# Performance work log

Hardware: AMD Instinct MI355X
Metric: run time of the kernel (lower is better)

The kernel has to match this reference:

```python
import jax, jax.numpy as jnp
import numpy as np

K = 5            # spline kernel size per dim
NUM_CLASSES = 10
EPS = 1e-4       # matches module's normalize eps
ROUTING_ITERS = 3
_BITS = jnp.array([[(b >> 2) & 1, (b >> 1) & 1, b & 1] for b in range(8)], dtype=jnp.float32)  # [8,3]


def normalize(t, axis=-1):
    return t / (jnp.sqrt(jnp.sum(t * t, axis=axis, keepdims=True)) + EPS)


def quat_mul(q, r):
    # quaternions stored (x, y, z, w) -- module sets identity as [:,:,:,3]=1
    qx, qy, qz, qw = q[..., 0], q[..., 1], q[..., 2], q[..., 3]
    rx, ry, rz, rw = r[..., 0], r[..., 1], r[..., 2], r[..., 3]
    return jnp.stack([
        qw * rx + qx * rw + qy * rz - qz * ry,
        qw * ry - qx * rz + qy * rw + qz * rx,
        qw * rz + qx * ry - qy * rx + qz * rw,
        qw * rw - qx * rx - qy * ry - qz * rz,
    ], axis=-1)


def spline_conv(x, pseudo, src, dst, W, root, bias, n_nodes):
    # degree-1 open B-spline conv, kernel 5^3, in=1, out=16
    v = pseudo * (K - 1)                                   # [E,3]
    i0 = jnp.clip(jnp.floor(v), 0, K - 2)                  # [E,3]
    frac = v - i0
    i0 = i0.astype(jnp.int32)
    idx = i0[:, None, :] + _BITS.astype(jnp.int32)[None]   # [E,8,3]
    kflat = (idx[..., 0] * K + idx[..., 1]) * K + idx[..., 2]  # [E,8]
    wb = jnp.prod(jnp.where(_BITS[None] > 0, frac[:, None, :], 1.0 - frac[:, None, :]), axis=-1)  # [E,8]
    Wg = W[kflat]                                          # [E,8,16] irregular gather (dominant traffic)
    wk = jnp.einsum('eb,ebo->eo', wb, Wg)                  # [E,16]
    msg = x[src] * wk                                      # [E,16] (in-channels = 1)
    agg = jax.ops.segment_sum(msg, dst, num_segments=n_nodes)
    deg = jax.ops.segment_sum(jnp.ones_like(dst, dtype=x.dtype), dst, num_segments=n_nodes)
    return agg / jnp.maximum(deg, 1.0)[:, None] + x @ root + bias


def caps_layer(pose, act, q):
    # pose [N,I,4], act [N,I], q [I,J,4] -> pose [N,J,4], act [N,J]
    qn = normalize(q)
    pred = normalize(quat_mul(qn[None], pose[:, :, None, :]))  # [N,I,J,4]
    b = jnp.zeros(pred.shape[:3], dtype=pose.dtype)
    for _ in range(ROUTING_ITERS):
        c = jax.nn.softmax(b, axis=2) * act[:, :, None]
        s = jnp.einsum('nij,nijq->njq', c, pred)
        v = normalize(s)
        b = b + jnp.einsum('nijq,njq->nij', pred, v)
    act_out = jax.nn.sigmoid(jnp.einsum('nij,nijq,njq->nj', c, pred, v))
    return v, act_out


def pool_by_agreement(pose, act, pos, G, start, size):
    # voxel-grid clustering + agreement-weighted quaternion averaging
    g = jnp.clip(jnp.floor((pos - start) / size), 0, G - 1).astype(jnp.int32)  # [N,3]
    vid = (g[:, 0] * G + g[:, 1]) * G + g[:, 2]
    V = G ** 3
    s = jax.ops.segment_sum(act[:, :, None] * pose, vid, num_segments=V)  # [V,J,4]
    m = normalize(s)
    agree = jnp.sum(pose * m[vid], axis=-1)                                # [N,J]
    wsum = jax.ops.segment_sum(act, vid, num_segments=V)
    cnt = jax.ops.segment_sum(jnp.ones((pose.shape[0],), pose.dtype), vid, num_segments=V)
    act_out = jax.nn.sigmoid(jax.ops.segment_sum(act * agree, vid, num_segments=V) / (wsum + EPS))
    pos_out = jax.ops.segment_sum(pos, vid, num_segments=V) / (cnt[:, None] + EPS)
    return m, act_out, pos_out


def forward(x, pos, pseudo, W_spline, root, bias, lin_w, lin_b, q0, q1, q3, q5, q6, q7, edge_index):
    N = x.shape[0]
    src, dst = edge_index[0], edge_index[1]
    h = spline_conv(x, pseudo, src, dst, W_spline, root, bias, N)   # [N,16]
    quats = jax.nn.elu(h) @ lin_w + lin_b                           # [N,4]
    pose = normalize(quats.reshape(N, 1, 4))                        # [N,1,4]
    act = x.reshape(N, 1)                                           # expand to num_caps_in=1
    pose, act = caps_layer(pose, act, q0)                           # 1 -> 6
    pose, act = caps_layer(pose, act, q1)                           # 6 -> 6
    min_pos, max_pos = pos.min(), pos.max()
    rng = max_pos + 0.001 - min_pos
    pose, act, p = pool_by_agreement(pose, act, pos, 32, min_pos, rng / 32)   # -> 32768 voxels
    pose, act = caps_layer(pose, act, q3)                           # 6 -> 8
    pose, act, p = pool_by_agreement(pose, act, p, 8, min_pos, rng / 8)       # -> 512
    pose, act = caps_layer(pose, act, q5)                           # 8 -> 12
    pose, act, p = pool_by_agreement(pose, act, p, 2, min_pos, rng / 2)       # -> 8
    pose, act = caps_layer(pose, act, q6)                           # 12 -> 14
    pose, act, p = pool_by_agreement(pose, act, p, 1, min_pos - 0.5, max_pos - min_pos + 1.0)  # -> 1
    pose, act = caps_layer(pose, act, q7)                           # 14 -> 10
    return act                                                      # [1, 10]


def setup_inputs() -> dict:
    key = jax.random.key(0)
    ks = jax.random.split(key, 16)
    N, E = 50000, 800000
    def caps_q(k, i, j):
        return jax.random.normal(k, (i, j, 4), dtype=jnp.float32)
    return {
        'x': jax.random.uniform(ks[0], (N, 1), dtype=jnp.float32),
        'pos': jax.random.uniform(ks[1], (N, 3), dtype=jnp.float32),
        'pseudo': jax.random.uniform(ks[2], (E, 3), dtype=jnp.float32),
        'W_spline': jax.random.normal(ks[3], (K ** 3, 16), dtype=jnp.float32) * 0.1,
        'root': jax.random.normal(ks[4], (1, 16), dtype=jnp.float32) * 0.1,
        'bias': jnp.zeros((16,), dtype=jnp.float32),
        'lin_w': jax.random.normal(ks[5], (16, 4), dtype=jnp.float32) * 0.25,
        'lin_b': jnp.zeros((4,), dtype=jnp.float32),
        'q0': caps_q(ks[6], 1, 6),
        'q1': caps_q(ks[7], 6, 6),
        'q3': caps_q(ks[8], 6, 8),
        'q5': caps_q(ks[9], 8, 12),
        'q6': caps_q(ks[10], 12, 14),
        'q7': caps_q(ks[11], 14, NUM_CLASSES),
        'edge_index': jax.random.randint(ks[12], (2, E), 0, N, dtype=jnp.int32),
    }


def reference(x, pos, pseudo, W_spline, root, bias, lin_w, lin_b, q0, q1, q3, q5, q6, q7, edge_index):
    return forward(x, pos, pseudo, W_spline, root, bias, lin_w, lin_b, q0, q1, q3, q5, q6, q7, edge_index)
```

## Files before the change

### kernel.cpp

```cpp
#include <hip/hip_runtime.h>
#include <math.h>

#define EPS 1e-4f

__device__ __forceinline__ float sigmoidf_(float x){ return 1.0f/(1.0f+expf(-x)); }

__device__ __forceinline__ unsigned f2u_(float f){
    unsigned u = __float_as_uint(f);
    return (u & 0x80000000u) ? ~u : (u | 0x80000000u);
}
__device__ __forceinline__ float u2f_(unsigned u){
    unsigned b = (u & 0x80000000u) ? (u & 0x7FFFFFFFu) : ~u;
    return __uint_as_float(b);
}

__global__ void minmax_kernel(const float* __restrict__ p, int n, unsigned* mm){
    float lo = INFINITY, hi = -INFINITY;
    for (int i = blockIdx.x*blockDim.x + threadIdx.x; i < n; i += gridDim.x*blockDim.x){
        float v = p[i]; lo = fminf(lo, v); hi = fmaxf(hi, v);
    }
    for (int off = 32; off > 0; off >>= 1){
        lo = fminf(lo, __shfl_down(lo, off));
        hi = fmaxf(hi, __shfl_down(hi, off));
    }
    __shared__ float slo[8], shi[8];
    int wid = threadIdx.x >> 6;
    if ((threadIdx.x & 63) == 0){ slo[wid] = lo; shi[wid] = hi; }
    __syncthreads();
    if (threadIdx.x == 0){
        int nw = blockDim.x >> 6;
        for (int w = 1; w < nw; w++){ lo = fminf(lo, slo[w]); hi = fmaxf(hi, shi[w]); }
        atomicMin(&mm[0], f2u_(lo));
        atomicMax(&mm[1], f2u_(hi));
    }
}

__global__ void edge_rank(const int* __restrict__ ei, int* __restrict__ deg,
                          int* __restrict__ rank, int E){
    int e = blockIdx.x*blockDim.x + threadIdx.x;
    if (e >= E) return;
    rank[e] = atomicAdd(&deg[ei[E + e]], 1);
}

__global__ __launch_bounds__(256)
void scan_bsum(const int* __restrict__ deg, int* __restrict__ bsum, int N){
    int i = blockIdx.x*256 + threadIdx.x;
    int v = (i < N) ? deg[i] : 0;
    for (int o = 32; o > 0; o >>= 1) v += __shfl_down(v, o);
    __shared__ int ws[4];
    if ((threadIdx.x & 63) == 0) ws[threadIdx.x >> 6] = v;
    __syncthreads();
    if (threadIdx.x == 0) bsum[blockIdx.x] = ws[0] + ws[1] + ws[2] + ws[3];
}

__global__ __launch_bounds__(1024)
void scan_top(int* __restrict__ bsum, int NB){
    __shared__ int sh[1024];
    int t = threadIdx.x;
    int v = (t < NB) ? bsum[t] : 0;
    sh[t] = v;
    __syncthreads();
    for (int d = 1; d < 1024; d <<= 1){
        int u = (t >= d) ? sh[t - d] : 0;
        __syncthreads();
        sh[t] += u;
        __syncthreads();
    }
    if (t < NB) bsum[t] = sh[t] - v;
    if (t == 1023) bsum[NB] = sh[1023];
}

__global__ __launch_bounds__(256)
void scan_final(const int* __restrict__ deg, const int* __restrict__ bsum,
                int* __restrict__ off, int N, int NB){
    __shared__ int sh[256];
    int b = blockIdx.x;
    int i = b*256 + threadIdx.x;
    int v = (i < N) ? deg[i] : 0;
    sh[threadIdx.x] = v;
    __syncthreads();
    for (int d = 1; d < 256; d <<= 1){
        int u = (threadIdx.x >= d) ? sh[threadIdx.x - d] : 0;
        __syncthreads();
        sh[threadIdx.x] += u;
        __syncthreads();
    }
    if (i < N) off[i] = bsum[b] + sh[threadIdx.x] - v;
    if (b == 0 && threadIdx.x == 0) off[N] = bsum[NB];
}

__global__ void edge_pack(const int* __restrict__ ei, const float* __restrict__ pseudo,
                          const float* __restrict__ x,
                          const int* __restrict__ rank, const int* __restrict__ off,
                          float4* __restrict__ rec4, int* __restrict__ recb, int E){
    int e = blockIdx.x*blockDim.x + threadIdx.x;
    if (e >= E) return;
    float p0 = pseudo[3*e], p1 = pseudo[3*e+1], p2 = pseudo[3*e+2];
    int s = ei[e], d = ei[E + e];
    float v0 = p0*4.f, v1 = p1*4.f, v2 = p2*4.f;
    float f0 = fminf(fmaxf(floorf(v0), 0.f), 3.f);
    float f1 = fminf(fmaxf(floorf(v1), 0.f), 3.f);
    float f2 = fminf(fmaxf(floorf(v2), 0.f), 3.f);
    int slot = off[d] + rank[e];
    rec4[slot] = make_float4(v0 - f0, v1 - f1, v2 - f2, x[s]);
    recb[slot] = ((int)f0*5 + (int)f1)*5 + (int)f2;
}

__device__ __forceinline__ int voxel_id(const float* __restrict__ pos, int n, int G,
                                        float start, float size){
    int g[3];
    #pragma unroll
    for (int k = 0; k < 3; k++){
        float gg = floorf((pos[(size_t)n*3 + k] - start) / size);
        gg = fminf(fmaxf(gg, 0.f), (float)(G - 1));
        g[k] = (int)gg;
    }
    return (g[0]*G + g[1])*G + g[2];
}

__device__ __forceinline__ void pool_geom(const unsigned* mm, int G, int mode,
                                          float& start, float& size){
    float mn = u2f_(mm[0]), mx = u2f_(mm[1]);
    if (mode == 0){ start = mn; size = (mx + 0.001f - mn) / (float)G; }
    else          { start = mn - 0.5f; size = mx - mn + 1.0f; }
}

__global__ void elist_node(const float* __restrict__ pos, int* __restrict__ head,
                           int* __restrict__ nxt, int N, int G, int mode,
                           const unsigned* __restrict__ mm){
    int n = blockIdx.x*blockDim.x + threadIdx.x;
    if (n >= N) return;
    float start, size; pool_geom(mm, G, mode, start, size);
    int v = voxel_id(pos, n, G, start, size);
    nxt[n] = atomicExch(&head[v], n);
}

__global__ __launch_bounds__(256)
void spline_node_kernel(const float* __restrict__ x, const float4* __restrict__ rec4,
                        const int* __restrict__ recb, const int* __restrict__ off,
                        const float* __restrict__ W,
                        const float* __restrict__ root, const float* __restrict__ bias,
                        const float* __restrict__ lin_w, const float* __restrict__ lin_b,
                        float* __restrict__ pose, float* __restrict__ act, int N){
    __shared__ float Ws[125*17];
    for (int i = threadIdx.x; i < 125*16; i += blockDim.x)
        Ws[(i >> 4)*17 + (i & 15)] = W[i];
    __syncthreads();
    int t = blockIdx.x*blockDim.x + threadIdx.x;
    int n = t >> 3;
    int k = t & 7;
    if (n >= N) return;

    int o0 = off[n], o1 = off[n+1];

    float agg[16];
    #pragma unroll
    for (int o = 0; o < 16; o++) agg[o] = 0.f;

    for (int s = o0 + k; s < o1; s += 8){
        float4 rv = rec4[s];
        int base = recb[s];
        float fr0 = rv.x, fr1 = rv.y, fr2 = rv.z, xv = rv.w;
        #pragma unroll
        for (int b = 0; b < 8; b++){
            int b0 = (b >> 2) & 1, b1 = (b >> 1) & 1, b2 = b & 1;
            float w = (b0 ? fr0 : 1.f - fr0) * (b1 ? fr1 : 1.f - fr1) * (b2 ? fr2 : 1.f - fr2);
            w *= xv;
            const float* Wr = &Ws[(base + b0*25 + b1*5 + b2)*17];
            #pragma unroll
            for (int o = 0; o < 16; o++) agg[o] += w * Wr[o];
        }
    }

    #pragma unroll
    for (int o = 0; o < 16; o++){
        agg[o] += __shfl_xor(agg[o], 1);
        agg[o] += __shfl_xor(agg[o], 2);
        agg[o] += __shfl_xor(agg[o], 4);
    }

    if (k != 0) return;

    float deg = fmaxf((float)(o1 - o0), 1.0f);
    float xs = x[n];
    float qv0 = lin_b[0], qv1 = lin_b[1], qv2 = lin_b[2], qv3 = lin_b[3];
    #pragma unroll
    for (int o = 0; o < 16; o++){
        float h = agg[o] / deg + xs * root[o] + bias[o];
        float e = (h > 0.f) ? h : expm1f(h);
        qv0 += e * lin_w[o*4 + 0];
        qv1 += e * lin_w[o*4 + 1];
        qv2 += e * lin_w[o*4 + 2];
        qv3 += e * lin_w[o*4 + 3];
    }
    float inv = 1.0f / (sqrtf(qv0*qv0 + qv1*qv1 + qv2*qv2 + qv3*qv3) + EPS);
    pose[(size_t)n*4 + 0] = qv0*inv;
    pose[(size_t)n*4 + 1] = qv1*inv;
    pose[(size_t)n*4 + 2] = qv2*inv;
    pose[(size_t)n*4 + 3] = qv3*inv;
    act[n] = xs;
}

template<int I, int J>
__global__ __launch_bounds__(256)
void caps_wave_kernel(const float* __restrict__ poseIn, const float* __restrict__ actIn,
                      const float* __restrict__ q,
                      float* __restrict__ poseOut, float* __restrict__ actOut, int N){
    __shared__ float qn[I*J*4];
    for (int t = threadIdx.x; t < I*J; t += blockDim.x){
        float qa=q[t*4], qb=q[t*4+1], qc=q[t*4+2], qd=q[t*4+3];
        float inv = 1.f/(sqrtf(qa*qa+qb*qb+qc*qc+qd*qd)+EPS);
        qn[t*4+0]=qa*inv; qn[t*4+1]=qb*inv; qn[t*4+2]=qc*inv; qn[t*4+3]=qd*inv;
    }
    __syncthreads();
    int tid = blockIdx.x*blockDim.x + threadIdx.x;
    int n = tid >> 3;
    int j = tid & 7;
    const bool on = (n < N) && (j < J);

    float pr[I][4], a[I], b[I];
    #pragma unroll
    for (int i = 0; i < I; i++){
        pr[i][0]=pr[i][1]=pr[i][2]=pr[i][3]=0.f; a[i]=0.f;
        b[i] = on ? 0.f : -INFINITY;
    }
    if (on){
        #pragma unroll
        for (int i = 0; i < I; i++){
            float4 p = *reinterpret_cast<const float4*>(&poseIn[((size_t)n*I + i)*4]);
            a[i] = actIn[(size_t)n*I + i];
            const float* qq = &qn[(i*J + j)*4];
            float qx=qq[0], qy=qq[1], qz=qq[2], qw=qq[3];
            float tx = qw*p.x + qx*p.w + qy*p.z - qz*p.y;
            float ty = qw*p.y - qx*p.z + qy*p.w + qz*p.x;
            float tz = qw*p.z + qx*p.y - qy*p.x + qz*p.w;
            float tw = qw*p.w - qx*p.x - qy*p.y - qz*p.z;
            float inv = 1.f/(sqrtf(tx*tx+ty*ty+tz*tz+tw*tw)+EPS);
            pr[i][0]=tx*inv; pr[i][1]=ty*inv; pr[i][2]=tz*inv; pr[i][3]=tw*inv;
        }
    }

    float c[I], v0=0.f, v1=0.f, v2=0.f, v3=0.f;
    #pragma unroll
    for (int t = 0; t < 3; t++){
        #pragma unroll
        for (int i = 0; i < I; i++){
            float mb = b[i];
            mb = fmaxf(mb, __shfl_xor(mb, 1));
            mb = fmaxf(mb, __shfl_xor(mb, 2));
            mb = fmaxf(mb, __shfl_xor(mb, 4));
            float e = on ? expf(b[i] - mb) : 0.f;
            float s = e;
            s += __shfl_xor(s, 1);
            s += __shfl_xor(s, 2);
            s += __shfl_xor(s, 4);
            c[i] = a[i] * e / s;
        }
        float s0=0.f, s1=0.f, s2=0.f, s3=0.f;
        #pragma unroll
        for (int i = 0; i < I; i++){
            s0 += c[i]*pr[i][0]; s1 += c[i]*pr[i][1];
            s2 += c[i]*pr[i][2]; s3 += c[i]*pr[i][3];
        }
        float inv = 1.f/(sqrtf(s0*s0+s1*s1+s2*s2+s3*s3)+EPS);
        v0=s0*inv; v1=s1*inv; v2=s2*inv; v3=s3*inv;
        if (t < 2){
            #pragma unroll
            for (int i = 0; i < I; i++)
                b[i] += pr[i][0]*v0 + pr[i][1]*v1 + pr[i][2]*v2 + pr[i][3]*v3;
        }
    }

    if (on){
        float acc = 0.f;
        #pragma unroll
        for (int i = 0; i < I; i++)
            acc += c[i]*(pr[i][0]*v0 + pr[i][1]*v1 + pr[i][2]*v2 + pr[i][3]*v3);
        actOut[(size_t)n*J + j] = sigmoidf_(acc);
        *reinterpret_cast<float4*>(&poseOut[((size_t)n*J + j)*4]) =
            make_float4(v0, v1, v2, v3);
    }
}

template<int I, int J, int NPB>
__global__ __launch_bounds__(NPB*I*J)
void caps_coop_kernel(const float* __restrict__ poseIn, const float* __restrict__ actIn,
                      const float* __restrict__ q, float* __restrict__ poseOut,
                      float* __restrict__ actOut, int N){
    const int IJ = I*J;
    const int tid = threadIdx.x;
    const int nl  = tid / IJ;
    const int li  = tid - nl*IJ;
    const int i   = li / J;
    const int j   = li - i*J;
    const int node = blockIdx.x*NPB + nl;
    const bool on = (node < N);

    __shared__ float redA[NPB][I*J];
    __shared__ float redB[NPB][I*J];
    __shared__ float cp[NPB][I*J*4];
    __shared__ float vsh[NPB][J*4];

    float prx=0.f, pry=0.f, prz=0.f, prw=0.f, ai=0.f;
    if (on){
        float qx = q[li*4+0], qy = q[li*4+1], qz = q[li*4+2], qw = q[li*4+3];
        float qinv = 1.0f/(sqrtf(qx*qx+qy*qy+qz*qz+qw*qw)+EPS);
        qx*=qinv; qy*=qinv; qz*=qinv; qw*=qinv;
        const float* pp = &poseIn[((size_t)node*I + i)*4];
        float rx=pp[0], ry=pp[1], rz=pp[2], rw=pp[3];
        ai = actIn[(size_t)node*I + i];
        float tx = qw*rx + qx*rw + qy*rz - qz*ry;
        float ty = qw*ry - qx*rz + qy*rw + qz*rx;
        float tz = qw*rz + qx*ry - qy*rx + qz*rw;
        float tw = qw*rw - qx*rx - qy*ry - qz*rz;
        float pinv = 1.0f/(sqrtf(tx*tx+ty*ty+tz*tz+tw*tw)+EPS);
        prx=tx*pinv; pry=ty*pinv; prz=tz*pinv; prw=tw*pinv;
    }

    float b = 0.f, c = 0.f;
    for (int t = 0; t < 3; t++){
        redA[nl][li] = b;
        __syncthreads();
        float mb = -INFINITY;
        #pragma unroll
        for (int jj = 0; jj < J; jj++) mb = fmaxf(mb, redA[nl][i*J+jj]);
        float e = expf(b - mb);
        redB[nl][li] = e;
        __syncthreads();
        float s = 0.f;
        #pragma unroll
        for (int jj = 0; jj < J; jj++) s += redB[nl][i*J+jj];
        c = ai * e / s;
        cp[nl][li*4+0] = c*prx; cp[nl][li*4+1] = c*pry;
        cp[nl][li*4+2] = c*prz; cp[nl][li*4+3] = c*prw;
        __syncthreads();
        for (int idx = li; idx < J*4; idx += IJ){
            int jj = idx >> 2, comp = idx & 3;
            float acc = 0.f;
            #pragma unroll
            for (int ii = 0; ii < I; ii++) acc += cp[nl][(ii*J+jj)*4+comp];
            vsh[nl][idx] = acc;
        }
        __syncthreads();
        if (li < J){
            float a0=vsh[nl][li*4], a1=vsh[nl][li*4+1], a2=vsh[nl][li*4+2], a3=vsh[nl][li*4+3];
            float inv = 1.0f/(sqrtf(a0*a0+a1*a1+a2*a2+a3*a3)+EPS);
            vsh[nl][li*4]=a0*inv; vsh[nl][li*4+1]=a1*inv;
            vsh[nl][li*4+2]=a2*inv; vsh[nl][li*4+3]=a3*inv;
        }
        __syncthreads();
        if (t < 2){
            b += prx*vsh[nl][j*4] + pry*vsh[nl][j*4+1] + prz*vsh[nl][j*4+2] + prw*vsh[nl][j*4+3];
            __syncthreads();
        } else {
            redA[nl][li] = c*(prx*vsh[nl][j*4] + pry*vsh[nl][j*4+1]
                            + prz*vsh[nl][j*4+2] + prw*vsh[nl][j*4+3]);
            __syncthreads();
            if (li < J && on){
                float acc = 0.f;
                #pragma unroll
                for (int ii = 0; ii < I; ii++) acc += redA[nl][ii*J+li];
                actOut[(size_t)node*J + li] = sigmoidf_(acc);
                poseOut[((size_t)node*J+li)*4+0] = vsh[nl][li*4+0];
                poseOut[((size_t)node*J+li)*4+1] = vsh[nl][li*4+1];
                poseOut[((size_t)node*J+li)*4+2] = vsh[nl][li*4+2];
                poseOut[((size_t)node*J+li)*4+3] = vsh[nl][li*4+3];
            }
        }
    }
}

template<int J>
__global__ __launch_bounds__(256)
void pool1_gather_kernel(const float* __restrict__ pose, const float* __restrict__ act,
                         const float* __restrict__ pos,
                         const int* __restrict__ head, const int* __restrict__ nxt,
                         float* __restrict__ poseOut, float* __restrict__ actOut,
                         float* __restrict__ posOut, int V){
    int v = blockIdx.x*blockDim.x + threadIdx.x;
    if (v >= V) return;

    float s[J][4], w[J], ps0=0.f, ps1=0.f, ps2=0.f;
    #pragma unroll
    for (int j = 0; j < J; j++){ s[j][0]=0.f; s[j][1]=0.f; s[j][2]=0.f; s[j][3]=0.f; w[j]=0.f; }

    int cnt = 0;
    for (int n = head[v]; n >= 0; n = nxt[n]){
        const float* pb = &pose[(size_t)n*J*4];
        const float* ab = &act[(size_t)n*J];
        #pragma unroll
        for (int j = 0; j < J; j++){
            float aj = ab[j];
            s[j][0] += aj*pb[j*4+0];
            s[j][1] += aj*pb[j*4+1];
            s[j][2] += aj*pb[j*4+2];
            s[j][3] += aj*pb[j*4+3];
            w[j] += aj;
        }
        ps0 += pos[(size_t)n*3+0];
        ps1 += pos[(size_t)n*3+1];
        ps2 += pos[(size_t)n*3+2];
        cnt++;
    }
    #pragma unroll
    for (int j = 0; j < J; j++){
        float inv = 1.0f/(sqrtf(s[j][0]*s[j][0]+s[j][1]*s[j][1]+
                                s[j][2]*s[j][2]+s[j][3]*s[j][3])+EPS);
        s[j][0]*=inv; s[j][1]*=inv; s[j][2]*=inv; s[j][3]*=inv;
    }
    float ag[J];
    #pragma unroll
    for (int j = 0; j < J; j++) ag[j] = 0.f;
    for (int n = head[v]; n >= 0; n = nxt[n]){
        const float* pb = &pose[(size_t)n*J*4];
        const float* ab = &act[(size_t)n*J];
        #pragma unroll
        for (int j = 0; j < J; j++){
            float agree = pb[j*4+0]*s[j][0] + pb[j*4+1]*s[j][1]
                        + pb[j*4+2]*s[j][2] + pb[j*4+3]*s[j][3];
            ag[j] += ab[j]*agree;
        }
    }
    #pragma unroll
    for (int j = 0; j < J; j++){
        size_t o = (size_t)v*J + j;
        actOut[o] = sigmoidf_(ag[j] / (w[j] + EPS));
        poseOut[o*4+0] = s[j][0];
        poseOut[o*4+1] = s[j][1];
        poseOut[o*4+2] = s[j][2];
        poseOut[o*4+3] = s[j][3];
    }
    float c = (float)cnt + EPS;
    posOut[(size_t)v*3+0] = ps0 / c;
    posOut[(size_t)v*3+1] = ps1 / c;
    posOut[(size_t)v*3+2] = ps2 / c;
}

template<int V, int J, int CH, int NCHUNK>
__global__ void pool_priv1(const float4* __restrict__ poseIn, const float* __restrict__ actIn,
                           const float* __restrict__ posIn,
                           float* __restrict__ s, float* __restrict__ wsum,
                           float* __restrict__ cnt, float* __restrict__ psum,
                           int N, int G, int mode, const unsigned* __restrict__ mm){
    __shared__ float s_[V*CH*4];
    __shared__ float wsum_[V*CH];
    __shared__ float cnt_[V];
    __shared__ float psum_[V*3];
    const int chunk = blockIdx.x % NCHUNK;
    const int slice = blockIdx.x / NCHUNK;
    const int nslices = gridDim.x / NCHUNK;
    const int c0 = chunk * CH;

    for (int t = threadIdx.x; t < V*CH*4; t += blockDim.x) s_[t] = 0.f;
    for (int t = threadIdx.x; t < V*CH; t += blockDim.x) wsum_[t] = 0.f;
    if (chunk == 0){
        for (int t = threadIdx.x; t < V; t += blockDim.x) cnt_[t] = 0.f;
        for (int t = threadIdx.x; t < V*3; t += blockDim.x) psum_[t] = 0.f;
    }
    __syncthreads();

    float start, size; pool_geom(mm, G, mode, start, size);
    int per = (N + nslices - 1) / nslices;
    int n0 = slice * per, n1 = min(N, n0 + per);

    for (int n = n0 + (int)threadIdx.x; n < n1; n += blockDim.x){
        int vid = voxel_id(posIn, n, G, start, size);
        #pragma unroll
        for (int jj = 0; jj < CH; jj++){
            int j = c0 + jj;
            float aj = actIn[(size_t)n*J + j];
            float4 p = poseIn[(size_t)n*J + j];
            int b = (vid*CH + jj)*4;
            atomicAdd(&s_[b+0], aj*p.x);
            atomicAdd(&s_[b+1], aj*p.y);
            atomicAdd(&s_[b+2], aj*p.z);
            atomicAdd(&s_[b+3], aj*p.w);
            atomicAdd(&wsum_[vid*CH + jj], aj);
        }
        if (chunk == 0){
            atomicAdd(&cnt_[vid], 1.0f);
            atomicAdd(&psum_[vid*3+0], posIn[(size_t)n*3+0]);
            atomicAdd(&psum_[vid*3+1], posIn[(size_t)n*3+1]);
            atomicAdd(&psum_[vid*3+2], posIn[(size_t)n*3+2]);
        }
    }
    __syncthreads();

    for (int t = threadIdx.x; t < V*CH*4; t += blockDim.x){
        float val = s_[t];
        if (val != 0.f){
            int v = t / (CH*4), r = t % (CH*4);
            atomicAdd(&s[((size_t)v*J + c0)*4 + r], val);
        }
    }
    for (int t = threadIdx.x; t < V*CH; t += blockDim.x){
        float val = wsum_[t];
        if (val != 0.f){
            int v = t / CH, jj = t % CH;
            atomicAdd(&wsum[(size_t)v*J + c0 + jj], val);
        }
    }
    if (chunk == 0){
        for (int t = threadIdx.x; t < V; t += blockDim.x)
            if (cnt_[t] != 0.f) atomicAdd(&cnt[t], cnt_[t]);
        for (int t = threadIdx.x; t < V*3; t += blockDim.x)
            if (psum_[t] != 0.f) atomicAdd(&psum[t], psum_[t]);
    }
}

template<int V, int J>
__global__ void pool_priv2(const float4* __restrict__ poseIn, const float* __restrict__ actIn,
                           const float* __restrict__ posIn, const float4* __restrict__ m,
                           float* __restrict__ agacc,
                           int N, int G, int mode, const unsigned* __restrict__ mm){
    __shared__ float ag_[V*J];
    for (int t = threadIdx.x; t < V*J; t += blockDim.x) ag_[t] = 0.f;
    __syncthreads();
    float start, size; pool_geom(mm, G, mode, start, size);
    int nslices = gridDim.x;
    int per = (N + nslices - 1) / nslices;
    int n0 = blockIdx.x * per, n1 = min(N, n0 + per);
    for (int n = n0 + (int)threadIdx.x; n < n1; n += blockDim.x){
        int vid = voxel_id(posIn, n, G, start, size);
        #pragma unroll
        for (int j = 0; j < J; j++){
            float4 p  = poseIn[(size_t)n*J + j];
            float4 mv = m[(size_t)vid*J + j];
            float agree = p.x*mv.x + p.y*mv.y + p.z*mv.z + p.w*mv.w;
            atomicAdd(&ag_[vid*J + j], actIn[(size_t)n*J + j]*agree);
        }
    }
    __syncthreads();
    for (int t = threadIdx.x; t < V*J; t += blockDim.x)
        if (ag_[t] != 0.f) atomicAdd(&agacc[t], ag_[t]);
}

__global__ void pool_m(const float* __restrict__ s, float* __restrict__ m, int VJ){
    int t = blockIdx.x*blockDim.x + threadIdx.x;
    if (t >= VJ) return;
    float a = s[(size_t)t*4], b = s[(size_t)t*4+1], c = s[(size_t)t*4+2], d = s[(size_t)t*4+3];
    float inv = 1.0f / (sqrtf(a*a + b*b + c*c + d*d) + EPS);
    m[(size_t)t*4]   = a*inv;
    m[(size_t)t*4+1] = b*inv;
    m[(size_t)t*4+2] = c*inv;
    m[(size_t)t*4+3] = d*inv;
}

__global__ void pool_fin(const float* __restrict__ agacc, const float* __restrict__ wsum,
                         const float* __restrict__ cnt, const float* __restrict__ psum,
                         float* __restrict__ actOut, float* __restrict__ posOut, int V, int J){
    int t = blockIdx.x*blockDim.x + threadIdx.x;
    if (t >= V*J) return;
    int v = t / J, j = t % J;
    actOut[t] = sigmoidf_(agacc[t] / (wsum[t] + EPS));
    if (j == 0){
        float c = cnt[v] + EPS;
        posOut[(size_t)v*3 + 0] = psum[(size_t)v*3 + 0] / c;
        posOut[(size_t)v*3 + 1] = psum[(size_t)v*3 + 1] / c;
        posOut[(size_t)v*3 + 2] = psum[(size_t)v*3 + 2] / c;
    }
}

template<int NIN, int J>
__global__ __launch_bounds__(64)
void pool4_tiny(const float* __restrict__ poseIn, const float* __restrict__ actIn,
                const float* __restrict__ posIn,
                float* __restrict__ poseOut, float* __restrict__ actOut,
                float* __restrict__ posOut){
    int t = threadIdx.x;
    if (t < J){
        float s0=0.f, s1=0.f, s2=0.f, s3=0.f, w=0.f;
        #pragma unroll
        for (int n = 0; n < NIN; n++){
            float a = actIn[n*J + t];
            const float* pb = &poseIn[(n*J + t)*4];
            s0 += a*pb[0]; s1 += a*pb[1]; s2 += a*pb[2]; s3 += a*pb[3];
            w += a;
        }
        float inv = 1.f/(sqrtf(s0*s0+s1*s1+s2*s2+s3*s3)+EPS);
        s0*=inv; s1*=inv; s2*=inv; s3*=inv;
        float ag = 0.f;
        #pragma unroll
        for (int n = 0; n < NIN; n++){
            float a = actIn[n*J + t];
            const float* pb = &poseIn[(n*J + t)*4];
            ag += a*(pb[0]*s0 + pb[1]*s1 + pb[2]*s2 + pb[3]*s3);
        }
        actOut[t] = sigmoidf_(ag / (w + EPS));
        poseOut[t*4+0]=s0; poseOut[t*4+1]=s1; poseOut[t*4+2]=s2; poseOut[t*4+3]=s3;
    } else if (t == J){
        float p0=0.f, p1=0.f, p2=0.f;
        #pragma unroll
        for (int n = 0; n < NIN; n++){
            p0 += posIn[n*3+0]; p1 += posIn[n*3+1]; p2 += posIn[n*3+2];
        }
        float c = (float)NIN + EPS;
        posOut[0]=p0/c; posOut[1]=p1/c; posOut[2]=p2/c;
    }
}

extern "C" void kernel_launch(void* const* d_in, const int* in_sizes, int n_in,
                              void* d_out, int out_size, void* d_ws, size_t ws_size,
                              hipStream_t stream){
    const float* x      = (const float*)d_in[0];
    const float* pos    = (const float*)d_in[1];
    const float* pseudo = (const float*)d_in[2];
    const float* Wsp    = (const float*)d_in[3];
    const float* root   = (const float*)d_in[4];
    const float* bias   = (const float*)d_in[5];
    const float* lin_w  = (const float*)d_in[6];
    const float* lin_b  = (const float*)d_in[7];
    const float* q0     = (const float*)d_in[8];
    const float* q1     = (const float*)d_in[9];
    const float* q3     = (const float*)d_in[10];
    const float* q5     = (const float*)d_in[11];
    const float* q6     = (const float*)d_in[12];
    const float* q7     = (const float*)d_in[13];
    const int*   ei     = (const int*)d_in[14];
    const int N = in_sizes[0];
    const int E = in_sizes[2] / 3;
    const int V1 = 32768;
    const int NB = (N + 255)/256;

    char* ws = (char*)d_ws;
    size_t off = 0;
    auto alloc = [&](size_t bytes)->void*{
        void* p = ws + off;
        off += (bytes + 255) & ~(size_t)255;
        return p;
    };
    unsigned* mm   = (unsigned*)alloc(8);
    int* deg       = (int*)alloc((size_t)N*sizeof(int));
    int* erank     = (int*)alloc((size_t)E*sizeof(int));
    int* eoff      = (int*)alloc((size_t)(N+1)*sizeof(int));
    int* bsum      = (int*)alloc((size_t)(NB+1)*sizeof(int));
    float4* rec4   = (float4*)alloc((size_t)E*sizeof(float4));
    int* recb      = (int*)alloc((size_t)E*sizeof(int));
    int* vhead     = (int*)alloc((size_t)V1*sizeof(int));
    int* vnxt      = (int*)alloc((size_t)N*sizeof(int));
    float* P0  = (float*)alloc((size_t)1250000*sizeof(float));
    float* P1  = (float*)alloc((size_t)1250000*sizeof(float));
    float* A0  = (float*)alloc((size_t)310000*sizeof(float));
    float* A1  = (float*)alloc((size_t)310000*sizeof(float));
    float* PB0 = (float*)alloc((size_t)100000*sizeof(float));
    float* PB1 = (float*)alloc((size_t)100000*sizeof(float));
    size_t pool_off0 = off;
    float* vs  = (float*)alloc((size_t)512*8*4*sizeof(float));
    float* vw  = (float*)alloc((size_t)512*8*sizeof(float));
    float* va  = (float*)alloc((size_t)512*8*sizeof(float));
    float* vc  = (float*)alloc((size_t)512*sizeof(float));
    float* vp  = (float*)alloc((size_t)512*3*sizeof(float));
    size_t pool_bytes = off - pool_off0;

    hipMemsetAsync(mm,     0xFF, 4, stream);
    hipMemsetAsync(mm + 1, 0x00, 4, stream);
    hipMemsetAsync(deg, 0, (size_t)N*sizeof(int), stream);
    hipMemsetAsync(vhead, 0xFF, (size_t)V1*sizeof(int), stream);

    minmax_kernel<<<80, 256, 0, stream>>>(pos, N*3, mm);

    edge_rank<<<(E + 255)/256, 256, 0, stream>>>(ei, deg, erank, E);
    scan_bsum<<<NB, 256, 0, stream>>>(deg, bsum, N);
    scan_top<<<1, 1024, 0, stream>>>(bsum, NB);
    scan_final<<<NB, 256, 0, stream>>>(deg, bsum, eoff, N, NB);
    edge_pack<<<(E + 255)/256, 256, 0, stream>>>(ei, pseudo, x, erank, eoff, rec4, recb, E);
    spline_node_kernel<<<(8*N + 255)/256, 256, 0, stream>>>(x, rec4, recb, eoff, Wsp,
                                                            root, bias, lin_w, lin_b, P0, A0, N);

    caps_wave_kernel<1,6><<<(8*N + 255)/256, 256, 0, stream>>>(P0, A0, q0, P1, A1, N);
    caps_wave_kernel<6,6><<<(8*N + 255)/256, 256, 0, stream>>>(P1, A1, q1, P0, A0, N);

    {
        const int G = 32;
        elist_node<<<(N + 255)/256, 256, 0, stream>>>(pos, vhead, vnxt, N, G, 0, mm);
        pool1_gather_kernel<6><<<(V1 + 255)/256, 256, 0, stream>>>(P0, A0, pos, vhead, vnxt,
                                                                   P1, A1, PB0, V1);
    }
    caps_wave_kernel<6,8><<<(8*32768 + 255)/256, 256, 0, stream>>>(P1, A1, q3, P0, A0, 32768);

    {
        const int V = 512, J = 8, G = 8, NSL = 64;
        hipMemsetAsync(vs, 0, pool_bytes, stream);
        pool_priv1<V,J,4,2><<<2*NSL, 256, 0, stream>>>((const float4*)P0, A0, PB0,
                                                       vs, vw, vc, vp, 32768, G, 0, mm);
        pool_m<<<(V*J + 255)/256, 256, 0, stream>>>(vs, P1, V*J);
        pool_priv2<V,J><<<NSL, 256, 0, stream>>>((const float4*)P0, A0, PB0,
                                                 (const float4*)P1, va, 32768, G, 0, mm);
        pool_fin<<<(V*J + 255)/256, 256, 0, stream>>>(va, vw, vc, vp, A1, PB1, V, J);
    }
    caps_coop_kernel<8,12,2><<<256, 2*96, 0, stream>>>(P1, A1, q5, P0, A0, 512);

    {
        const int V = 8, J = 12, G = 2, NSL = 16;
        hipMemsetAsync(vs, 0, pool_bytes, stream);
        pool_priv1<V,J,12,1><<<NSL, 256, 0, stream>>>((const float4*)P0, A0, PB1,
                                                      vs, vw, vc, vp, 512, G, 0, mm);
        pool_m<<<1, 256, 0, stream>>>(vs, P1, V*J);
        pool_priv2<V,J><<<NSL, 256, 0, stream>>>((const float4*)P0, A0, PB1,
                                                 (const float4*)P1, va, 512, G, 0, mm);
        pool_fin<<<1, 256, 0, stream>>>(va, vw, vc, vp, A1, PB0, V, J);
    }
    caps_coop_kernel<12,14,1><<<8, 168, 0, stream>>>(P1, A1, q6, P0, A0, 8);

    pool4_tiny<8,14><<<1, 64, 0, stream>>>(P0, A0, PB0, P1, A1, PB1);
    caps_coop_kernel<14,10,1><<<1, 140, 0, stream>>>(P1, A1, q7, P0, (float*)d_out, 1);
}
```

Measured before the change: 332.5 us.

## Fuse capsule stages with pooling and merge init launches to cut kernel count

The separate memsets, minmax and edge-rank launches become one init kernel and one prep kernel. The first two capsule layers run in one kernel that also builds the voxel linked list, and the first pooling gather is fused with the next capsule layer. Pool finalization is folded into the capsule kernels, and the last pool is merged with the final capsule layer. The aim is to remove launch overhead and intermediate global round trips. The cost is larger kernels with more register pressure and a grid-stride prep kernel that may run with less parallelism.

```diff
diff --git a/kernel.cpp b/kernel.cpp
--- a/kernel.cpp
+++ b/kernel.cpp
@@ -14,32 +14,41 @@
     return __uint_as_float(b);
 }
 
-__global__ void minmax_kernel(const float* __restrict__ p, int n, unsigned* mm){
+__global__ void init_kernel(unsigned* __restrict__ mm, int* __restrict__ deg, int N,
+                            int* __restrict__ vhead, int V,
+                            float* __restrict__ pz, int PZ){
+    int i = blockIdx.x*blockDim.x + threadIdx.x;
+    int stride = gridDim.x*blockDim.x;
+    if (i == 0){ mm[0] = 0xFFFFFFFFu; mm[1] = 0u; }
+    for (int t = i; t < N; t += stride) deg[t] = 0;
+    for (int t = i; t < V; t += stride) vhead[t] = -1;
+    for (int t = i; t < PZ; t += stride) pz[t] = 0.f;
+}
+
+__global__ void prep_kernel(const float* __restrict__ p, int n3, unsigned* mm,
+                            const int* __restrict__ ei, int* __restrict__ deg,
+                            int* __restrict__ rank, int E){
+    int gid = blockIdx.x*blockDim.x + threadIdx.x;
+    int stride = gridDim.x*blockDim.x;
     float lo = INFINITY, hi = -INFINITY;
-    for (int i = blockIdx.x*blockDim.x + threadIdx.x; i < n; i += gridDim.x*blockDim.x){
+    for (int i = gid; i < n3; i += stride){
         float v = p[i]; lo = fminf(lo, v); hi = fmaxf(hi, v);
     }
     for (int off = 32; off > 0; off >>= 1){
         lo = fminf(lo, __shfl_down(lo, off));
         hi = fmaxf(hi, __shfl_down(hi, off));
     }
-    __shared__ float slo[8], shi[8];
+    __shared__ float slo[4], shi[4];
     int wid = threadIdx.x >> 6;
     if ((threadIdx.x & 63) == 0){ slo[wid] = lo; shi[wid] = hi; }
     __syncthreads();
     if (threadIdx.x == 0){
-        int nw = blockDim.x >> 6;
-        for (int w = 1; w < nw; w++){ lo = fminf(lo, slo[w]); hi = fmaxf(hi, shi[w]); }
+        for (int w = 1; w < 4; w++){ lo = fminf(lo, slo[w]); hi = fmaxf(hi, shi[w]); }
         atomicMin(&mm[0], f2u_(lo));
         atomicMax(&mm[1], f2u_(hi));
     }
-}
-
-__global__ void edge_rank(const int* __restrict__ ei, int* __restrict__ deg,
-                          int* __restrict__ rank, int E){
-    int e = blockIdx.x*blockDim.x + threadIdx.x;
-    if (e >= E) return;
-    rank[e] = atomicAdd(&deg[ei[E + e]], 1);
+    for (int e = gid; e < E; e += stride)
+        rank[e] = atomicAdd(&deg[ei[E + e]], 1);
 }
 
 __global__ __launch_bounds__(256)
@@ -125,16 +134,6 @@
     else          { start = mn - 0.5f; size = mx - mn + 1.0f; }
 }
 
-__global__ void elist_node(const float* __restrict__ pos, int* __restrict__ head,
-                           int* __restrict__ nxt, int N, int G, int mode,
-                           const unsigned* __restrict__ mm){
-    int n = blockIdx.x*blockDim.x + threadIdx.x;
-    if (n >= N) return;
-    float start, size; pool_geom(mm, G, mode, start, size);
-    int v = voxel_id(pos, n, G, start, size);
-    nxt[n] = atomicExch(&head[v], n);
-}
-
 __global__ __launch_bounds__(256)
 void spline_node_kernel(const float* __restrict__ x, const float4* __restrict__ rec4,
                         const int* __restrict__ recb, const int* __restrict__ off,
@@ -201,46 +200,25 @@
     act[n] = xs;
 }
 
-template<int I, int J>
-__global__ __launch_bounds__(256)
-void caps_wave_kernel(const float* __restrict__ poseIn, const float* __restrict__ actIn,
-                      const float* __restrict__ q,
-                      float* __restrict__ poseOut, float* __restrict__ actOut, int N){
-    __shared__ float qn[I*J*4];
-    for (int t = threadIdx.x; t < I*J; t += blockDim.x){
-        float qa=q[t*4], qb=q[t*4+1], qc=q[t*4+2], qd=q[t*4+3];
-        float inv = 1.f/(sqrtf(qa*qa+qb*qb+qc*qc+qd*qd)+EPS);
-        qn[t*4+0]=qa*inv; qn[t*4+1]=qb*inv; qn[t*4+2]=qc*inv; qn[t*4+3]=qd*inv;
-    }
-    __syncthreads();
-    int tid = blockIdx.x*blockDim.x + threadIdx.x;
-    int n = tid >> 3;
-    int j = tid & 7;
-    const bool on = (n < N) && (j < J);
-
-    float pr[I][4], a[I], b[I];
-    #pragma unroll
-    for (int i = 0; i < I; i++){
-        pr[i][0]=pr[i][1]=pr[i][2]=pr[i][3]=0.f; a[i]=0.f;
-        b[i] = on ? 0.f : -INFINITY;
-    }
-    if (on){
-        #pragma unroll
-        for (int i = 0; i < I; i++){
-            float4 p = *reinterpret_cast<const float4*>(&poseIn[((size_t)n*I + i)*4]);
-            a[i] = actIn[(size_t)n*I + i];
-            const float* qq = &qn[(i*J + j)*4];
-            float qx=qq[0], qy=qq[1], qz=qq[2], qw=qq[3];
-            float tx = qw*p.x + qx*p.w + qy*p.z - qz*p.y;
-            float ty = qw*p.y - qx*p.z + qy*p.w + qz*p.x;
-            float tz = qw*p.z + qx*p.y - qy*p.x + qz*p.w;
-            float tw = qw*p.w - qx*p.x - qy*p.y - qz*p.z;
-            float inv = 1.f/(sqrtf(tx*tx+ty*ty+tz*tz+tw*tw)+EPS);
-            pr[i][0]=tx*inv; pr[i][1]=ty*inv; pr[i][2]=tz*inv; pr[i][3]=tw*inv;
-        }
-    }
-
-    float c[I], v0=0.f, v1=0.f, v2=0.f, v3=0.f;
+__device__ __forceinline__ void quat_pred(const float* qq, float px, float py, float pz,
+                                          float pw, float* pr){
+    float qx=qq[0], qy=qq[1], qz=qq[2], qw=qq[3];
+    float tx = qw*px + qx*pw + qy*pz - qz*py;
+    float ty = qw*py - qx*pz + qy*pw + qz*px;
+    float tz = qw*pz + qx*py - qy*px + qz*pw;
+    float tw = qw*pw - qx*px - qy*py - qz*pz;
+    float inv = 1.f/(sqrtf(tx*tx+ty*ty+tz*tz+tw*tw)+EPS);
+    pr[0]=tx*inv; pr[1]=ty*inv; pr[2]=tz*inv; pr[3]=tw*inv;
+}
+
+template<int I>
+__device__ __forceinline__ void caps_route8(const float (*pr)[4], const float* a, bool on,
+                                            float* c, float& v0, float& v1,
+                                            float& v2, float& v3){
+    float b[I];
+    #pragma unroll
+    for (int i = 0; i < I; i++) b[i] = on ? 0.f : -INFINITY;
+    v0=v1=v2=v3=0.f;
     #pragma unroll
     for (int t = 0; t < 3; t++){
         #pragma unroll
@@ -270,23 +248,276 @@
                 b[i] += pr[i][0]*v0 + pr[i][1]*v1 + pr[i][2]*v2 + pr[i][3]*v3;
         }
     }
-
+}
+
+__global__ __launch_bounds__(256)
+void caps01_kernel(const float* __restrict__ pose0, const float* __restrict__ act0,
+                   const float* __restrict__ q0, const float* __restrict__ q1,
+                   float* __restrict__ poseOut, float* __restrict__ actOut,
+                   const float* __restrict__ pos, int* __restrict__ vhead,
+                   int* __restrict__ vnxt, int N, int G,
+                   const unsigned* __restrict__ mm){
+    __shared__ float qn0[6*4], qn1[36*4];
+    for (int t = threadIdx.x; t < 6; t += blockDim.x){
+        float qa=q0[t*4],qb=q0[t*4+1],qc=q0[t*4+2],qd=q0[t*4+3];
+        float inv=1.f/(sqrtf(qa*qa+qb*qb+qc*qc+qd*qd)+EPS);
+        qn0[t*4]=qa*inv; qn0[t*4+1]=qb*inv; qn0[t*4+2]=qc*inv; qn0[t*4+3]=qd*inv;
+    }
+    for (int t = threadIdx.x; t < 36; t += blockDim.x){
+        float qa=q1[t*4],qb=q1[t*4+1],qc=q1[t*4+2],qd=q1[t*4+3];
+        float inv=1.f/(sqrtf(qa*qa+qb*qb+qc*qc+qd*qd)+EPS);
+        qn1[t*4]=qa*inv; qn1[t*4+1]=qb*inv; qn1[t*4+2]=qc*inv; qn1[t*4+3]=qd*inv;
+    }
+    __syncthreads();
+    int tid = blockIdx.x*blockDim.x + threadIdx.x;
+    int n = tid >> 3, j = tid & 7;
+    if (n >= N) return;
+    bool on = (j < 6);
+
+    float4 p0 = *reinterpret_cast<const float4*>(&pose0[(size_t)n*4]);
+    float aa0[1] = { act0[n] };
+    float pr0[1][4] = {{0.f,0.f,0.f,0.f}};
+    if (on) quat_pred(&qn0[j*4], p0.x, p0.y, p0.z, p0.w, pr0[0]);
+    float c0[1], v0x, v0y, v0z, v0w;
+    caps_route8<1>(pr0, aa0, on, c0, v0x, v0y, v0z, v0w);
+    float al0 = sigmoidf_(c0[0]*(pr0[0][0]*v0x + pr0[0][1]*v0y
+                                + pr0[0][2]*v0z + pr0[0][3]*v0w));
+
+    float pi[6][4], ai[6];
+    #pragma unroll
+    for (int i = 0; i < 6; i++){
+        pi[i][0] = __shfl(v0x, i, 8);
+        pi[i][1] = __shfl(v0y, i, 8);
+        pi[i][2] = __shfl(v0z, i, 8);
+        pi[i][3] = __shfl(v0w, i, 8);
+        ai[i]    = __shfl(al0, i, 8);
+    }
+
+    float pr[6][4];
+    #pragma unroll
+    for (int i = 0; i < 6; i++){
+        pr[i][0]=pr[i][1]=pr[i][2]=pr[i][3]=0.f;
+        if (on) quat_pred(&qn1[(i*6+j)*4], pi[i][0], pi[i][1], pi[i][2], pi[i][3], pr[i]);
+    }
+    float c1[6], v1x, v1y, v1z, v1w;
+    caps_route8<6>(pr, ai, on, c1, v1x, v1y, v1z, v1w);
     if (on){
         float acc = 0.f;
         #pragma unroll
-        for (int i = 0; i < I; i++)
-            acc += c[i]*(pr[i][0]*v0 + pr[i][1]*v1 + pr[i][2]*v2 + pr[i][3]*v3);
-        actOut[(size_t)n*J + j] = sigmoidf_(acc);
-        *reinterpret_cast<float4*>(&poseOut[((size_t)n*J + j)*4]) =
-            make_float4(v0, v1, v2, v3);
+        for (int i = 0; i < 6; i++)
+            acc += c1[i]*(pr[i][0]*v1x + pr[i][1]*v1y + pr[i][2]*v1z + pr[i][3]*v1w);
+        actOut[(size_t)n*6 + j] = sigmoidf_(acc);
+        *reinterpret_cast<float4*>(&poseOut[((size_t)n*6 + j)*4]) =
+            make_float4(v1x, v1y, v1z, v1w);
+    }
+    if (j == 0){
+        float start, size; pool_geom(mm, G, 0, start, size);
+        int vid = voxel_id(pos, n, G, start, size);
+        vnxt[n] = atomicExch(&vhead[vid], n);
+    }
+}
+
+__global__ __launch_bounds__(256)
+void pool1caps_kernel(const float* __restrict__ poseIn, const float* __restrict__ actIn,
+                      const float* __restrict__ pos,
+                      const int* __restrict__ head, const int* __restrict__ nxt,
+                      const float* __restrict__ q3,
+                      float* __restrict__ poseOut, float* __restrict__ actOut,
+                      float* __restrict__ posOut, int V){
+    __shared__ float qn[48*4];
+    for (int t = threadIdx.x; t < 48; t += blockDim.x){
+        float qa=q3[t*4],qb=q3[t*4+1],qc=q3[t*4+2],qd=q3[t*4+3];
+        float inv=1.f/(sqrtf(qa*qa+qb*qb+qc*qc+qd*qd)+EPS);
+        qn[t*4]=qa*inv; qn[t*4+1]=qb*inv; qn[t*4+2]=qc*inv; qn[t*4+3]=qd*inv;
+    }
+    __syncthreads();
+    int tid = blockIdx.x*blockDim.x + threadIdx.x;
+    int v = tid >> 3, j = tid & 7;
+    if (v >= V) return;
+    bool onj = (j < 6);
+
+    float s0=0.f,s1=0.f,s2=0.f,s3=0.f, w=0.f, ps0=0.f,ps1=0.f,ps2=0.f;
+    int cnt = 0;
+    for (int n = head[v]; n >= 0; n = nxt[n]){
+        if (onj){
+            float aj = actIn[(size_t)n*6 + j];
+            float4 pb = *reinterpret_cast<const float4*>(&poseIn[((size_t)n*6 + j)*4]);
+            s0 += aj*pb.x; s1 += aj*pb.y; s2 += aj*pb.z; s3 += aj*pb.w;
+            w += aj;
+        } else if (j == 6){
+            ps0 += pos[(size_t)n*3+0]; ps1 += pos[(size_t)n*3+1]; ps2 += pos[(size_t)n*3+2];
+        }
+        cnt++;
+    }
+    float m0=0.f,m1=0.f,m2=0.f,m3=0.f;
+    if (onj){
+        float inv = 1.f/(sqrtf(s0*s0+s1*s1+s2*s2+s3*s3)+EPS);
+        m0=s0*inv; m1=s1*inv; m2=s2*inv; m3=s3*inv;
+    }
+    float ag = 0.f;
+    for (int n = head[v]; n >= 0; n = nxt[n]){
+        if (onj){
+            float aj = actIn[(size_t)n*6 + j];
+            float4 pb = *reinterpret_cast<const float4*>(&poseIn[((size_t)n*6 + j)*4]);
+            ag += aj*(pb.x*m0 + pb.y*m1 + pb.z*m2 + pb.w*m3);
+        }
+    }
+    float actm = sigmoidf_(ag/(w+EPS));
+    if (j == 6){
+        float c = (float)cnt + EPS;
+        posOut[(size_t)v*3+0] = ps0/c;
+        posOut[(size_t)v*3+1] = ps1/c;
+        posOut[(size_t)v*3+2] = ps2/c;
+    }
+
+    float pi[6][4], ai[6];
+    #pragma unroll
+    for (int i = 0; i < 6; i++){
+        pi[i][0] = __shfl(m0, i, 8);
+        pi[i][1] = __shfl(m1, i, 8);
+        pi[i][2] = __shfl(m2, i, 8);
+        pi[i][3] = __shfl(m3, i, 8);
+        ai[i]    = __shfl(actm, i, 8);
+    }
+    float pr[6][4];
+    #pragma unroll
+    for (int i = 0; i < 6; i++)
+        quat_pred(&qn[(i*8+j)*4], pi[i][0], pi[i][1], pi[i][2], pi[i][3], pr[i]);
+    float c1[6], vx, vy, vz, vw;
+    caps_route8<6>(pr, ai, true, c1, vx, vy, vz, vw);
+    float acc = 0.f;
+    #pragma unroll
+    for (int i = 0; i < 6; i++)
+        acc += c1[i]*(pr[i][0]*vx + pr[i][1]*vy + pr[i][2]*vz + pr[i][3]*vw);
+    actOut[(size_t)v*8 + j] = sigmoidf_(acc);
+    *reinterpret_cast<float4*>(&poseOut[((size_t)v*8 + j)*4]) = make_float4(vx, vy, vz, vw);
+}
+
+template<int V, int J, int CH, int NCHUNK>
+__global__ void pool_priv1(const float4* __restrict__ poseIn, const float* __restrict__ actIn,
+                           const float* __restrict__ posIn,
+                           float* __restrict__ s, float* __restrict__ wsum,
+                           float* __restrict__ cnt, float* __restrict__ psum,
+                           int N, int G, int mode, const unsigned* __restrict__ mm){
+    __shared__ float s_[V*CH*4];
+    __shared__ float wsum_[V*CH];
+    __shared__ float cnt_[V];
+    __shared__ float psum_[V*3];
+    const int chunk = blockIdx.x % NCHUNK;
+    const int slice = blockIdx.x / NCHUNK;
+    const int nslices = gridDim.x / NCHUNK;
+    const int c0 = chunk * CH;
+
+    for (int t = threadIdx.x; t < V*CH*4; t += blockDim.x) s_[t] = 0.f;
+    for (int t = threadIdx.x; t < V*CH; t += blockDim.x) wsum_[t] = 0.f;
+    if (chunk == 0){
+        for (int t = threadIdx.x; t < V; t += blockDim.x) cnt_[t] = 0.f;
+        for (int t = threadIdx.x; t < V*3; t += blockDim.x) psum_[t] = 0.f;
+    }
+    __syncthreads();
+
+    float start, size; pool_geom(mm, G, mode, start, size);
+    int per = (N + nslices - 1) / nslices;
+    int n0 = slice * per, n1 = min(N, n0 + per);
+
+    for (int n = n0 + (int)threadIdx.x; n < n1; n += blockDim.x){
+        int vid = voxel_id(posIn, n, G, start, size);
+        #pragma unroll
+        for (int jj = 0; jj < CH; jj++){
+            int j = c0 + jj;
+            float aj = actIn[(size_t)n*J + j];
+            float4 p = poseIn[(size_t)n*J + j];
+            int b = (vid*CH + jj)*4;
+            atomicAdd(&s_[b+0], aj*p.x);
+            atomicAdd(&s_[b+1], aj*p.y);
+            atomicAdd(&s_[b+2], aj*p.z);
+            atomicAdd(&s_[b+3], aj*p.w);
+            atomicAdd(&wsum_[vid*CH + jj], aj);
+        }
+        if (chunk == 0){
+            atomicAdd(&cnt_[vid], 1.0f);
+            atomicAdd(&psum_[vid*3+0], posIn[(size_t)n*3+0]);
+            atomicAdd(&psum_[vid*3+1], posIn[(size_t)n*3+1]);
+            atomicAdd(&psum_[vid*3+2], posIn[(size_t)n*3+2]);
+        }
+    }
+    __syncthreads();
+
+    for (int t = threadIdx.x; t < V*CH*4; t += blockDim.x){
+        float val = s_[t];
+        if (val != 0.f){
+            int v = t / (CH*4), r = t % (CH*4);
+            atomicAdd(&s[((size_t)v*J + c0)*4 + r], val);
+        }
+    }
+    for (int t = threadIdx.x; t < V*CH; t += blockDim.x){
+        float val = wsum_[t];
+        if (val != 0.f){
+            int v = t / CH, jj = t % CH;
+            atomicAdd(&wsum[(size_t)v*J + c0 + jj], val);
+        }
+    }
+    if (chunk == 0){
+        for (int t = threadIdx.x; t < V; t += blockDim.x)
+            if (cnt_[t] != 0.f) atomicAdd(&cnt[t], cnt_[t]);
+        for (int t = threadIdx.x; t < V*3; t += blockDim.x)
+            if (psum_[t] != 0.f) atomicAdd(&psum[t], psum_[t]);
+    }
+}
+
+template<int V, int J>
+__global__ void pool_priv2(const float4* __restrict__ poseIn, const float* __restrict__ actIn,
+                           const float* __restrict__ posIn, const float4* __restrict__ m,
+                           float* __restrict__ agacc,
+                           int N, int G, int mode, const unsigned* __restrict__ mm){
+    __shared__ float ag_[V*J];
+    for (int t = threadIdx.x; t < V*J; t += blockDim.x) ag_[t] = 0.f;
+    __syncthreads();
+    float start, size; pool_geom(mm, G, mode, start, size);
+    int nslices = gridDim.x;
+    int per = (N + nslices - 1) / nslices;
+    int n0 = blockIdx.x * per, n1 = min(N, n0 + per);
+    for (int n = n0 + (int)threadIdx.x; n < n1; n += blockDim.x){
+        int vid = voxel_id(posIn, n, G, start, size);
+        #pragma unroll
+        for (int j = 0; j < J; j++){
+            float4 p  = poseIn[(size_t)n*J + j];
+            float4 mv = m[(size_t)vid*J + j];
+            float agree = p.x*mv.x + p.y*mv.y + p.z*mv.z + p.w*mv.w;
+            atomicAdd(&ag_[vid*J + j], actIn[(size_t)n*J + j]*agree);
+        }
+    }
+    __syncthreads();
+    for (int t = threadIdx.x; t < V*J; t += blockDim.x)
+        if (ag_[t] != 0.f) atomicAdd(&agacc[t], ag_[t]);
+}
+
+__global__ void pool_m2(const float* __restrict__ s, float* __restrict__ m,
+                        const float* __restrict__ cnt, const float* __restrict__ psum,
+                        float* __restrict__ posOut, int V, int J){
+    int t = blockIdx.x*blockDim.x + threadIdx.x;
+    if (t < V*J){
+        float a = s[(size_t)t*4], b = s[(size_t)t*4+1];
+        float c = s[(size_t)t*4+2], d = s[(size_t)t*4+3];
+        float inv = 1.0f / (sqrtf(a*a + b*b + c*c + d*d) + EPS);
+        m[(size_t)t*4]   = a*inv;
+        m[(size_t)t*4+1] = b*inv;
+        m[(size_t)t*4+2] = c*inv;
+        m[(size_t)t*4+3] = d*inv;
+    }
+    if (t < V){
+        float c = cnt[t] + EPS;
+        posOut[(size_t)t*3+0] = psum[(size_t)t*3+0] / c;
+        posOut[(size_t)t*3+1] = psum[(size_t)t*3+1] / c;
+        posOut[(size_t)t*3+2] = psum[(size_t)t*3+2] / c;
     }
 }
 
 template<int I, int J, int NPB>
 __global__ __launch_bounds__(NPB*I*J)
-void caps_coop_kernel(const float* __restrict__ poseIn, const float* __restrict__ actIn,
-                      const float* __restrict__ q, float* __restrict__ poseOut,
-                      float* __restrict__ actOut, int N){
+void caps_coop_fin(const float* __restrict__ poseIn, const float* __restrict__ agacc,
+                   const float* __restrict__ wsum, const float* __restrict__ q,
+                   float* __restrict__ poseOut, float* __restrict__ actOut, int N){
     const int IJ = I*J;
     const int tid = threadIdx.x;
     const int nl  = tid / IJ;
@@ -308,7 +539,7 @@
         qx*=qinv; qy*=qinv; qz*=qinv; qw*=qinv;
         const float* pp = &poseIn[((size_t)node*I + i)*4];
         float rx=pp[0], ry=pp[1], rz=pp[2], rw=pp[3];
-        ai = actIn[(size_t)node*I + i];
+        ai = sigmoidf_(agacc[(size_t)node*I + i] / (wsum[(size_t)node*I + i] + EPS));
         float tx = qw*rx + qx*rw + qy*rz - qz*ry;
         float ty = qw*ry - qx*rz + qy*rw + qz*rx;
         float tz = qw*rz + qx*ry - qy*rx + qz*rw;
@@ -370,210 +601,19 @@
     }
 }
 
-template<int J>
-__global__ __launch_bounds__(256)
-void pool1_gather_kernel(const float* __restrict__ pose, const float* __restrict__ act,
-                         const float* __restrict__ pos,
-                         const int* __restrict__ head, const int* __restrict__ nxt,
-                         float* __restrict__ poseOut, float* __restrict__ actOut,
-                         float* __restrict__ posOut, int V){
-    int v = blockIdx.x*blockDim.x + threadIdx.x;
-    if (v >= V) return;
-
-    float s[J][4], w[J], ps0=0.f, ps1=0.f, ps2=0.f;
-    #pragma unroll
-    for (int j = 0; j < J; j++){ s[j][0]=0.f; s[j][1]=0.f; s[j][2]=0.f; s[j][3]=0.f; w[j]=0.f; }
-
-    int cnt = 0;
-    for (int n = head[v]; n >= 0; n = nxt[n]){
-        const float* pb = &pose[(size_t)n*J*4];
-        const float* ab = &act[(size_t)n*J];
-        #pragma unroll
-        for (int j = 0; j < J; j++){
-            float aj = ab[j];
-            s[j][0] += aj*pb[j*4+0];
-            s[j][1] += aj*pb[j*4+1];
-            s[j][2] += aj*pb[j*4+2];
-            s[j][3] += aj*pb[j*4+3];
-            w[j] += aj;
-        }
-        ps0 += pos[(size_t)n*3+0];
-        ps1 += pos[(size_t)n*3+1];
-        ps2 += pos[(size_t)n*3+2];
-        cnt++;
-    }
-    #pragma unroll
-    for (int j = 0; j < J; j++){
-        float inv = 1.0f/(sqrtf(s[j][0]*s[j][0]+s[j][1]*s[j][1]+
-                                s[j][2]*s[j][2]+s[j][3]*s[j][3])+EPS);
-        s[j][0]*=inv; s[j][1]*=inv; s[j][2]*=inv; s[j][3]*=inv;
-    }
-    float ag[J];
-    #pragma unroll
-    for (int j = 0; j < J; j++) ag[j] = 0.f;
-    for (int n = head[v]; n >= 0; n = nxt[n]){
-        const float* pb = &pose[(size_t)n*J*4];
-        const float* ab = &act[(size_t)n*J];
-        #pragma unroll
-        for (int j = 0; j < J; j++){
-            float agree = pb[j*4+0]*s[j][0] + pb[j*4+1]*s[j][1]
-                        + pb[j*4+2]*s[j][2] + pb[j*4+3]*s[j][3];
-            ag[j] += ab[j]*agree;
-        }
-    }
-    #pragma unroll
-    for (int j = 0; j < J; j++){
-        size_t o = (size_t)v*J + j;
-        actOut[o] = sigmoidf_(ag[j] / (w[j] + EPS));
-        poseOut[o*4+0] = s[j][0];
-        poseOut[o*4+1] = s[j][1];
-        poseOut[o*4+2] = s[j][2];
-        poseOut[o*4+3] = s[j][3];
-    }
-    float c = (float)cnt + EPS;
-    posOut[(size_t)v*3+0] = ps0 / c;
-    posOut[(size_t)v*3+1] = ps1 / c;
-    posOut[(size_t)v*3+2] = ps2 / c;
-}
-
-template<int V, int J, int CH, int NCHUNK>
-__global__ void pool_priv1(const float4* __restrict__ poseIn, const float* __restrict__ actIn,
-                           const float* __restrict__ posIn,
-                           float* __restrict__ s, float* __restrict__ wsum,
-                           float* __restrict__ cnt, float* __restrict__ psum,
-                           int N, int G, int mode, const unsigned* __restrict__ mm){
-    __shared__ float s_[V*CH*4];
-    __shared__ float wsum_[V*CH];
-    __shared__ float cnt_[V];
-    __shared__ float psum_[V*3];
-    const int chunk = blockIdx.x % NCHUNK;
-    const int slice = blockIdx.x / NCHUNK;
-    const int nslices = gridDim.x / NCHUNK;
-    const int c0 = chunk * CH;
-
-    for (int t = threadIdx.x; t < V*CH*4; t += blockDim.x) s_[t] = 0.f;
-    for (int t = threadIdx.x; t < V*CH; t += blockDim.x) wsum_[t] = 0.f;
-    if (chunk == 0){
-        for (int t = threadIdx.x; t < V; t += blockDim.x) cnt_[t] = 0.f;
-        for (int t = threadIdx.x; t < V*3; t += blockDim.x) psum_[t] = 0.f;
-    }
-    __syncthreads();
-
-    float start, size; pool_geom(mm, G, mode, start, size);
-    int per = (N + nslices - 1) / nslices;
-    int n0 = slice * per, n1 = min(N, n0 + per);
-
-    for (int n = n0 + (int)threadIdx.x; n < n1; n += blockDim.x){
-        int vid = voxel_id(posIn, n, G, start, size);
-        #pragma unroll
-        for (int jj = 0; jj < CH; jj++){
-            int j = c0 + jj;
-            float aj = actIn[(size_t)n*J + j];
-            float4 p = poseIn[(size_t)n*J + j];
-            int b = (vid*CH + jj)*4;
-            atomicAdd(&s_[b+0], aj*p.x);
-            atomicAdd(&s_[b+1], aj*p.y);
-            atomicAdd(&s_[b+2], aj*p.z);
-            atomicAdd(&s_[b+3], aj*p.w);
-            atomicAdd(&wsum_[vid*CH + jj], aj);
-        }
-        if (chunk == 0){
-            atomicAdd(&cnt_[vid], 1.0f);
-            atomicAdd(&psum_[vid*3+0], posIn[(size_t)n*3+0]);
-            atomicAdd(&psum_[vid*3+1], posIn[(size_t)n*3+1]);
-            atomicAdd(&psum_[vid*3+2], posIn[(size_t)n*3+2]);
-        }
-    }
-    __syncthreads();
-
-    for (int t = threadIdx.x; t < V*CH*4; t += blockDim.x){
-        float val = s_[t];
-        if (val != 0.f){
-            int v = t / (CH*4), r = t % (CH*4);
-            atomicAdd(&s[((size_t)v*J + c0)*4 + r], val);
-        }
-    }
-    for (int t = threadIdx.x; t < V*CH; t += blockDim.x){
-        float val = wsum_[t];
-        if (val != 0.f){
-            int v = t / CH, jj = t % CH;
-            atomicAdd(&wsum[(size_t)v*J + c0 + jj], val);
-        }
-    }
-    if (chunk == 0){
-        for (int t = threadIdx.x; t < V; t += blockDim.x)
-            if (cnt_[t] != 0.f) atomicAdd(&cnt[t], cnt_[t]);
-        for (int t = threadIdx.x; t < V*3; t += blockDim.x)
-            if (psum_[t] != 0.f) atomicAdd(&psum[t], psum_[t]);
-    }
-}
-
-template<int V, int J>
-__global__ void pool_priv2(const float4* __restrict__ poseIn, const float* __restrict__ actIn,
-                           const float* __restrict__ posIn, const float4* __restrict__ m,
-                           float* __restrict__ agacc,
-                           int N, int G, int mode, const unsigned* __restrict__ mm){
-    __shared__ float ag_[V*J];
-    for (int t = threadIdx.x; t < V*J; t += blockDim.x) ag_[t] = 0.f;
-    __syncthreads();
-    float start, size; pool_geom(mm, G, mode, start, size);
-    int nslices = gridDim.x;
-    int per = (N + nslices - 1) / nslices;
-    int n0 = blockIdx.x * per, n1 = min(N, n0 + per);
-    for (int n = n0 + (int)threadIdx.x; n < n1; n += blockDim.x){
-        int vid = voxel_id(posIn, n, G, start, size);
-        #pragma unroll
-        for (int j = 0; j < J; j++){
-            float4 p  = poseIn[(size_t)n*J + j];
-            float4 mv = m[(size_t)vid*J + j];
-            float agree = p.x*mv.x + p.y*mv.y + p.z*mv.z + p.w*mv.w;
-            atomicAdd(&ag_[vid*J + j], actIn[(size_t)n*J + j]*agree);
-        }
-    }
-    __syncthreads();
-    for (int t = threadIdx.x; t < V*J; t += blockDim.x)
-        if (ag_[t] != 0.f) atomicAdd(&agacc[t], ag_[t]);
-}
-
-__global__ void pool_m(const float* __restrict__ s, float* __restrict__ m, int VJ){
-    int t = blockIdx.x*blockDim.x + threadIdx.x;
-    if (t >= VJ) return;
-    float a = s[(size_t)t*4], b = s[(size_t)t*4+1], c = s[(size_t)t*4+2], d = s[(size_t)t*4+3];
-    float inv = 1.0f / (sqrtf(a*a + b*b + c*c + d*d) + EPS);
-    m[(size_t)t*4]   = a*inv;
-    m[(size_t)t*4+1] = b*inv;
-    m[(size_t)t*4+2] = c*inv;
-    m[(size_t)t*4+3] = d*inv;
-}
-
-__global__ void pool_fin(const float* __restrict__ agacc, const float* __restrict__ wsum,
-                         const float* __restrict__ cnt, const float* __restrict__ psum,
-                         float* __restrict__ actOut, float* __restrict__ posOut, int V, int J){
-    int t = blockIdx.x*blockDim.x + threadIdx.x;
-    if (t >= V*J) return;
-    int v = t / J, j = t % J;
-    actOut[t] = sigmoidf_(agacc[t] / (wsum[t] + EPS));
-    if (j == 0){
-        float c = cnt[v] + EPS;
-        posOut[(size_t)v*3 + 0] = psum[(size_t)v*3 + 0] / c;
-        posOut[(size_t)v*3 + 1] = psum[(size_t)v*3 + 1] / c;
-        posOut[(size_t)v*3 + 2] = psum[(size_t)v*3 + 2] / c;
-    }
-}
-
-template<int NIN, int J>
-__global__ __launch_bounds__(64)
-void pool4_tiny(const float* __restrict__ poseIn, const float* __restrict__ actIn,
-                const float* __restrict__ posIn,
-                float* __restrict__ poseOut, float* __restrict__ actOut,
-                float* __restrict__ posOut){
+__global__ __launch_bounds__(192)
+void pool4final_kernel(const float* __restrict__ poseIn, const float* __restrict__ actIn,
+                       const float* __restrict__ q7, float* __restrict__ out){
+    const int NIN = 8, JP = 14, I = 14, J = 10;
+    __shared__ float mp[JP*4], ma[JP];
+    __shared__ float redA[I*J], redB[I*J], cp[I*J*4], vsh[J*4];
     int t = threadIdx.x;
-    if (t < J){
-        float s0=0.f, s1=0.f, s2=0.f, s3=0.f, w=0.f;
+    if (t < JP){
+        float s0=0.f,s1=0.f,s2=0.f,s3=0.f,w=0.f;
         #pragma unroll
         for (int n = 0; n < NIN; n++){
-            float a = actIn[n*J + t];
-            const float* pb = &poseIn[(n*J + t)*4];
+            float a = actIn[n*JP + t];
+            const float* pb = &poseIn[(n*JP + t)*4];
             s0 += a*pb[0]; s1 += a*pb[1]; s2 += a*pb[2]; s3 += a*pb[3];
             w += a;
         }
@@ -582,20 +622,81 @@
         float ag = 0.f;
         #pragma unroll
         for (int n = 0; n < NIN; n++){
-            float a = actIn[n*J + t];
-            const float* pb = &poseIn[(n*J + t)*4];
+            float a = actIn[n*JP + t];
+            const float* pb = &poseIn[(n*JP + t)*4];
             ag += a*(pb[0]*s0 + pb[1]*s1 + pb[2]*s2 + pb[3]*s3);
         }
-        actOut[t] = sigmoidf_(ag / (w + EPS));
-        poseOut[t*4+0]=s0; poseOut[t*4+1]=s1; poseOut[t*4+2]=s2; poseOut[t*4+3]=s3;
-    } else if (t == J){
-        float p0=0.f, p1=0.f, p2=0.f;
-        #pragma unroll
-        for (int n = 0; n < NIN; n++){
-            p0 += posIn[n*3+0]; p1 += posIn[n*3+1]; p2 += posIn[n*3+2];
-        }
-        float c = (float)NIN + EPS;
-        posOut[0]=p0/c; posOut[1]=p1/c; posOut[2]=p2/c;
+        ma[t] = sigmoidf_(ag / (w + EPS));
+        mp[t*4+0]=s0; mp[t*4+1]=s1; mp[t*4+2]=s2; mp[t*4+3]=s3;
+    }
+    __syncthreads();
+
+    bool act_thr = (t < I*J);
+    int li = act_thr ? t : 0;
+    int i = li / J, j = li % J;
+    float prx=0.f, pry=0.f, prz=0.f, prw=0.f, ai=0.f;
+    if (act_thr){
+        float qx=q7[li*4],qy=q7[li*4+1],qz=q7[li*4+2],qw=q7[li*4+3];
+        float qinv = 1.f/(sqrtf(qx*qx+qy*qy+qz*qz+qw*qw)+EPS);
+        qx*=qinv; qy*=qinv; qz*=qinv; qw*=qinv;
+        float rx=mp[i*4], ry=mp[i*4+1], rz=mp[i*4+2], rw=mp[i*4+3];
+        ai = ma[i];
+        float tx = qw*rx + qx*rw + qy*rz - qz*ry;
+        float ty = qw*ry - qx*rz + qy*rw + qz*rx;
+        float tz = qw*rz + qx*ry - qy*rx + qz*rw;
+        float tw = qw*rw - qx*rx - qy*ry - qz*rz;
+        float pinv = 1.f/(sqrtf(tx*tx+ty*ty+tz*tz+tw*tw)+EPS);
+        prx=tx*pinv; pry=ty*pinv; prz=tz*pinv; prw=tw*pinv;
+    }
+    float b = 0.f, c = 0.f;
+    for (int it = 0; it < 3; it++){
+        if (act_thr) redA[li] = b;
+        __syncthreads();
+        float mb = -INFINITY;
+        #pragma unroll
+        for (int jj = 0; jj < J; jj++) mb = fmaxf(mb, redA[i*J+jj]);
+        float e = expf(b - mb);
+        if (act_thr) redB[li] = e;
+        __syncthreads();
+        float s = 0.f;
+        #pragma unroll
+        for (int jj = 0; jj < J; jj++) s += redB[i*J+jj];
+        c = ai * e / s;
+        if (act_thr){
+            cp[li*4+0]=c*prx; cp[li*4+1]=c*pry; cp[li*4+2]=c*prz; cp[li*4+3]=c*prw;
+        }
+        __syncthreads();
+        if (act_thr){
+            for (int idx = li; idx < J*4; idx += I*J){
+                int jj = idx >> 2, comp = idx & 3;
+                float acc = 0.f;
+                #pragma unroll
+                for (int ii = 0; ii < I; ii++) acc += cp[(ii*J+jj)*4+comp];
+                vsh[idx] = acc;
+            }
+        }
+        __syncthreads();
+        if (act_thr && li < J){
+            float a0=vsh[li*4], a1=vsh[li*4+1], a2=vsh[li*4+2], a3=vsh[li*4+3];
+            float inv = 1.f/(sqrtf(a0*a0+a1*a1+a2*a2+a3*a3)+EPS);
+            vsh[li*4]=a0*inv; vsh[li*4+1]=a1*inv; vsh[li*4+2]=a2*inv; vsh[li*4+3]=a3*inv;
+        }
+        __syncthreads();
+        if (it < 2){
+            b += prx*vsh[j*4] + pry*vsh[j*4+1] + prz*vsh[j*4+2] + prw*vsh[j*4+3];
+            __syncthreads();
+        } else {
+            if (act_thr)
+                redA[li] = c*(prx*vsh[j*4] + pry*vsh[j*4+1]
+                            + prz*vsh[j*4+2] + prw*vsh[j*4+3]);
+            __syncthreads();
+            if (act_thr && li < J){
+                float acc = 0.f;
+                #pragma unroll
+                for (int ii = 0; ii < I; ii++) acc += redA[ii*J+li];
+                out[li] = sigmoidf_(acc);
+            }
+        }
     }
 }
 
@@ -644,22 +745,23 @@
     float* A1  = (float*)alloc((size_t)310000*sizeof(float));
     float* PB0 = (float*)alloc((size_t)100000*sizeof(float));
     float* PB1 = (float*)alloc((size_t)100000*sizeof(float));
-    size_t pool_off0 = off;
-    float* vs  = (float*)alloc((size_t)512*8*4*sizeof(float));
-    float* vw  = (float*)alloc((size_t)512*8*sizeof(float));
-    float* va  = (float*)alloc((size_t)512*8*sizeof(float));
-    float* vc  = (float*)alloc((size_t)512*sizeof(float));
-    float* vp  = (float*)alloc((size_t)512*3*sizeof(float));
-    size_t pool_bytes = off - pool_off0;
-
-    hipMemsetAsync(mm,     0xFF, 4, stream);
-    hipMemsetAsync(mm + 1, 0x00, 4, stream);
-    hipMemsetAsync(deg, 0, (size_t)N*sizeof(int), stream);
-    hipMemsetAsync(vhead, 0xFF, (size_t)V1*sizeof(int), stream);
-
-    minmax_kernel<<<80, 256, 0, stream>>>(pos, N*3, mm);
-
-    edge_rank<<<(E + 255)/256, 256, 0, stream>>>(ei, deg, erank, E);
+    size_t z0 = off;
+    float* vs2 = (float*)alloc((size_t)512*8*4*sizeof(float));
+    float* vw2 = (float*)alloc((size_t)512*8*sizeof(float));
+    float* va2 = (float*)alloc((size_t)512*8*sizeof(float));
+    float* vc2 = (float*)alloc((size_t)512*sizeof(float));
+    float* vp2 = (float*)alloc((size_t)512*3*sizeof(float));
+    float* vs3 = (float*)alloc((size_t)8*12*4*sizeof(float));
+    float* vw3 = (float*)alloc((size_t)8*12*sizeof(float));
+    float* va3 = (float*)alloc((size_t)8*12*sizeof(float));
+    float* vc3 = (float*)alloc((size_t)8*sizeof(float));
+    float* vp3 = (float*)alloc((size_t)8*3*sizeof(float));
+    size_t z1 = off;
+    float* pzero = (float*)(ws + z0);
+    const int PZ = (int)((z1 - z0)/sizeof(float));
+
+    init_kernel<<<256, 256, 0, stream>>>(mm, deg, N, vhead, V1, pzero, PZ);
+    prep_kernel<<<512, 256, 0, stream>>>(pos, N*3, mm, ei, deg, erank, E);
     scan_bsum<<<NB, 256, 0, stream>>>(deg, bsum, N);
     scan_top<<<1, 1024, 0, stream>>>(bsum, NB);
     scan_final<<<NB, 256, 0, stream>>>(deg, bsum, eoff, N, NB);
@@ -667,41 +769,24 @@
     spline_node_kernel<<<(8*N + 255)/256, 256, 0, stream>>>(x, rec4, recb, eoff, Wsp,
                                                             root, bias, lin_w, lin_b, P0, A0, N);
 
-    caps_wave_kernel<1,6><<<(8*N + 255)/256, 256, 0, stream>>>(P0, A0, q0, P1, A1, N);
-    caps_wave_kernel<6,6><<<(8*N + 255)/256, 256, 0, stream>>>(P1, A1, q1, P0, A0, N);
-
-    {
-        const int G = 32;
-        elist_node<<<(N + 255)/256, 256, 0, stream>>>(pos, vhead, vnxt, N, G, 0, mm);
-        pool1_gather_kernel<6><<<(V1 + 255)/256, 256, 0, stream>>>(P0, A0, pos, vhead, vnxt,
-                                                                   P1, A1, PB0, V1);
-    }
-    caps_wave_kernel<6,8><<<(8*32768 + 255)/256, 256, 0, stream>>>(P1, A1, q3, P0, A0, 32768);
-
-    {
-        const int V = 512, J = 8, G = 8, NSL = 64;
-        hipMemsetAsync(vs, 0, pool_bytes, stream);
-        pool_priv1<V,J,4,2><<<2*NSL, 256, 0, stream>>>((const float4*)P0, A0, PB0,
-                                                       vs, vw, vc, vp, 32768, G, 0, mm);
-        pool_m<<<(V*J + 255)/256, 256, 0, stream>>>(vs, P1, V*J);
-        pool_priv2<V,J><<<NSL, 256, 0, stream>>>((const float4*)P0, A0, PB0,
-                                                 (const float4*)P1, va, 32768, G, 0, mm);
-        pool_fin<<<(V*J + 255)/256, 256, 0, stream>>>(va, vw, vc, vp, A1, PB1, V, J);
-    }
-    caps_coop_kernel<8,12,2><<<256, 2*96, 0, stream>>>(P1, A1, q5, P0, A0, 512);
-
-    {
-        const int V = 8, J = 12, G = 2, NSL = 16;
-        hipMemsetAsync(vs, 0, pool_bytes, stream);
-        pool_priv1<V,J,12,1><<<NSL, 256, 0, stream>>>((const float4*)P0, A0, PB1,
-                                                      vs, vw, vc, vp, 512, G, 0, mm);
-        pool_m<<<1, 256, 0, stream>>>(vs, P1, V*J);
-        pool_priv2<V,J><<<NSL, 256, 0, stream>>>((const float4*)P0, A0, PB1,
-                                                 (const float4*)P1, va, 512, G, 0, mm);
-        pool_fin<<<1, 256, 0, stream>>>(va, vw, vc, vp, A1, PB0, V, J);
-    }
-    caps_coop_kernel<12,14,1><<<8, 168, 0, stream>>>(P1, A1, q6, P0, A0, 8);
-
-    pool4_tiny<8,14><<<1, 64, 0, stream>>>(P0, A0, PB0, P1, A1, PB1);
-    caps_coop_kernel<14,10,1><<<1, 140, 0, stream>>>(P1, A1, q7, P0, (float*)d_out, 1);
-}
+    caps01_kernel<<<(8*N + 255)/256, 256, 0, stream>>>(P0, A0, q0, q1, P1, A1,
+                                                       pos, vhead, vnxt, N, 32, mm);
+    pool1caps_kernel<<<(8*V1 + 255)/256, 256, 0, stream>>>(P1, A1, pos, vhead, vnxt,
+                                                           q3, P0, A0, PB0, V1);
+
+    pool_priv1<512,8,4,2><<<128, 256, 0, stream>>>((const float4*)P0, A0, PB0,
+                                                   vs2, vw2, vc2, vp2, 32768, 8, 0, mm);
+    pool_m2<<<16, 256, 0, stream>>>(vs2, P1, vc2, vp2, PB1, 512, 8);
+    pool_priv2<512,8><<<64, 256, 0, stream>>>((const float4*)P0, A0, PB0,
+                                              (const float4*)P1, va2, 32768, 8, 0, mm);
+    caps_coop_fin<8,12,2><<<256, 2*96, 0, stream>>>(P1, va2, vw2, q5, P0, A0, 512);
+
+    pool_priv1<8,12,12,1><<<16, 256, 0, stream>>>((const float4*)P0, A0, PB1,
+                                                  vs3, vw3, vc3, vp3, 512, 2, 0, mm);
+    pool_m2<<<1, 256, 0, stream>>>(vs3, P1, vc3, vp3, PB0, 8, 12);
+    pool_priv2<8,12><<<16, 256, 0, stream>>>((const float4*)P0, A0, PB1,
+                                             (const float4*)P1, va3, 512, 2, 0, mm);
+    caps_coop_fin<12,14,1><<<8, 168, 0, stream>>>(P1, va3, vw3, q6, P0, A0, 8);
+
+    pool4final_kernel<<<1, 192, 0, stream>>>(P0, A0, q7, (float*)d_out);
+}
```

Measured after the change: 309.3 us. -7.0%, faster.
